# Performance work log

Hardware: AMD Instinct MI355X
Metric: run time of the kernel (lower is better)

The kernel has to match this reference:

```python
import jax, jax.numpy as jnp
import numpy as np

WS = 8          # window_size
NH = 4          # num_heads
C = 128         # embed_dim
HD = C // NH    # head_dim
HID = 4 * C     # mlp hidden
EPS = 1e-5


def _rel_pos_index(ws):
    coords = np.stack(np.meshgrid(np.arange(ws), np.arange(ws), indexing='ij')).reshape(2, -1)
    rel = coords[:, :, None] - coords[:, None, :]          # (2, N, N)
    rel = rel.transpose(1, 2, 0).astype(np.int64)          # (N, N, 2)
    rel[..., 0] += ws - 1
    rel[..., 1] += ws - 1
    rel[..., 0] *= 2 * ws - 1
    return rel.sum(-1)                                     # (N, N)


def _layernorm(x, g, b):
    mu = jnp.mean(x, axis=-1, keepdims=True)
    var = jnp.mean(jnp.square(x - mu), axis=-1, keepdims=True)
    return (x - mu) * jax.lax.rsqrt(var + EPS) * g + b


def setup_inputs() -> dict:
    key = jax.random.key(0)
    ks = jax.random.split(key, 12)
    B, L = 32, 4096
    s = 0.02
    return {
        'x': jax.random.normal(ks[0], (B, L, C), jnp.float32),
        'W_qkv': jax.random.normal(ks[1], (C, 3 * C), jnp.float32) * s,
        'b_qkv': jnp.zeros((3 * C,), jnp.float32),
        'W_out': jax.random.normal(ks[2], (C, C), jnp.float32) * s,
        'b_out': jnp.zeros((C,), jnp.float32),
        'bias_table': jax.random.normal(ks[3], ((2 * WS - 1) ** 2, NH), jnp.float32) * s,
        'g1': jnp.ones((C,), jnp.float32), 'be1': jnp.zeros((C,), jnp.float32),
        'g2': jnp.ones((C,), jnp.float32), 'be2': jnp.zeros((C,), jnp.float32),
        'W_fc1': jax.random.normal(ks[4], (C, HID), jnp.float32) * s,
        'b_fc1': jnp.zeros((HID,), jnp.float32),
        'W_fc2': jax.random.normal(ks[5], (HID, C), jnp.float32) * s,
        'b_fc2': jnp.zeros((C,), jnp.float32),
        'H': 64, 'W': 64,
    }


def reference(x, W_qkv, b_qkv, W_out, b_out, bias_table, g1, be1, g2, be2,
              W_fc1, b_fc1, W_fc2, b_fc2, H, W):
    B, L, _ = x.shape
    N = WS * WS
    shortcut = x
    xn = _layernorm(x, g1, be1)
    # window partition: (B,H,W,C) -> (B*nw, N, C)
    xw = xn.reshape(B, H // WS, WS, W // WS, WS, C)
    xw = xw.transpose(0, 1, 3, 2, 4, 5).reshape(-1, N, C)
    # attention
    qkv = (xw @ W_qkv + b_qkv).reshape(-1, N, 3, NH, HD)
    q, k, v = jnp.moveaxis(qkv, 2, 0)                      # each (Bw, N, NH, HD)
    attn = jnp.einsum('bnhd,bmhd->bhnm', q, k) * (HD ** -0.5)
    idx = jnp.asarray(_rel_pos_index(WS))                  # (N, N)
    bias = bias_table[idx].transpose(2, 0, 1)              # (NH, N, N)
    attn = jax.nn.softmax((attn + bias[None]).astype(jnp.float32), axis=-1).astype(x.dtype)
    o = jnp.einsum('bhnm,bmhd->bnhd', attn, v).reshape(-1, N, C)
    o = o @ W_out + b_out
    # window reverse
    o = o.reshape(B, H // WS, W // WS, WS, WS, C)
    o = o.transpose(0, 1, 3, 2, 4, 5).reshape(B, L, C)
    x = shortcut + o
    # MLP block
    xn = _layernorm(x, g2, be2)
    h = jax.nn.gelu(xn @ W_fc1 + b_fc1, approximate=False)
    return x + (h @ W_fc2 + b_fc2)
```

## Files before the change

### kernel.cpp

```cpp
#include <hip/hip_runtime.h>
#include <hip/hip_bf16.h>

typedef __bf16 bf16;
typedef __bf16 bf16x8 __attribute__((ext_vector_type(8)));
typedef __bf16 bf16x4 __attribute__((ext_vector_type(4)));
typedef float f32x4 __attribute__((ext_vector_type(4)));

#define C_DIM 128
#define LDA 136
#define LDQ 40
#define LDVT 72
#define LDP 72
#define LDH 264

__device__ __forceinline__ f32x4 mfma16(bf16x8 a, bf16x8 b, f32x4 c) {
  return __builtin_amdgcn_mfma_f32_16x16x32_bf16(a, b, c, 0, 0, 0);
}


__global__ __launch_bounds__(256, 2) void swin_fused(
    const float* __restrict__ x,
    const bf16*  __restrict__ Wqkv_t, const float* __restrict__ b_qkv,
    const bf16*  __restrict__ Wout_t, const float* __restrict__ b_out,
    const float* __restrict__ btabx,
    const float* __restrict__ g1, const float* __restrict__ be1,
    const float* __restrict__ g2, const float* __restrict__ be2,
    const bf16*  __restrict__ Wfc1_t, const float* __restrict__ b_fc1,
    const bf16*  __restrict__ Wfc2_t, const float* __restrict__ b_fc2,
    float* __restrict__ out)
{
  __shared__ __attribute__((aligned(16))) char smem[76800];
  bf16 (*sA)[LDA]       = (bf16(*)[LDA])(smem);
  bf16 (*sQ)[64][LDQ]   = (bf16(*)[64][LDQ])(smem + 17408);
  bf16 (*sK)[64][LDQ]   = (bf16(*)[64][LDQ])(smem + 37888);
  bf16 (*sVT)[32][LDVT] = (bf16(*)[32][LDVT])(smem + 58368);
  bf16 (*sP)[64][LDP]   = (bf16(*)[64][LDP])(smem + 17408);
  bf16 (*sY)[LDA]       = (bf16(*)[LDA])(smem + 17408);
  bf16 (*sH)[LDH]       = (bf16(*)[LDH])(smem + 17408);

  const int tid = threadIdx.x;
  const int w   = tid >> 6;
  const int l   = tid & 63;
  const int l15 = l & 15;
  const int lhi = l >> 4;

  const int win = blockIdx.x;
  const int b   = win >> 6;
  const int wy  = (win >> 3) & 7;
  const int wx  = win & 7;
  const int rowbase = b * 4096 + wy * 512 + wx * 8;

  f32x4 yreg[2][4];

  {
    const int tok = tid >> 2, seg = tid & 3;
    const int t = rowbase + (tok >> 3) * 64 + (tok & 7);
    const float* xr = x + (size_t)t * C_DIM + seg * 32;
    float f[32]; float s = 0.f, s2 = 0.f;
    #pragma unroll
    for (int i = 0; i < 8; i++) {
      f32x4 v = *(const f32x4*)(xr + i * 4);
      #pragma unroll
      for (int j = 0; j < 4; j++) { float a = v[j]; f[i*4+j] = a; s += a; s2 += a*a; }
    }
    s  += __shfl_xor(s, 1);  s  += __shfl_xor(s, 2);
    s2 += __shfl_xor(s2, 1); s2 += __shfl_xor(s2, 2);
    float mu = s * (1.f/128.f);
    float rs = rsqrtf(s2 * (1.f/128.f) - mu*mu + 1e-5f);
    #pragma unroll
    for (int i = 0; i < 4; i++) {
      f32x4 gv0 = *(const f32x4*)(g1  + seg*32 + i*8);
      f32x4 gv1 = *(const f32x4*)(g1  + seg*32 + i*8 + 4);
      f32x4 bv0 = *(const f32x4*)(be1 + seg*32 + i*8);
      f32x4 bv1 = *(const f32x4*)(be1 + seg*32 + i*8 + 4);
      bf16x8 o;
      #pragma unroll
      for (int j = 0; j < 4; j++) {
        o[j]   = (bf16)((f[i*8+j]   - mu) * rs * gv0[j] + bv0[j]);
        o[j+4] = (bf16)((f[i*8+j+4] - mu) * rs * gv1[j] + bv1[j]);
      }
      *(bf16x8*)&sA[tok][seg*32 + i*8] = o;
    }
  }
  __syncthreads();

  {
    bf16x8 a[4][4];
    #pragma unroll
    for (int mt = 0; mt < 4; mt++)
      #pragma unroll
      for (int ks = 0; ks < 4; ks++)
        a[mt][ks] = *(const bf16x8*)&sA[mt*16 + l15][ks*32 + lhi*8];
    const float scale = 0.17677669529663687f;
    #pragma unroll
    for (int nti = 0; nti < 6; nti++) {
      const int kind  = nti >> 1;
      const int dhalf = nti & 1;
      const int colg_l = kind*128 + w*32 + dhalf*16 + l15;
      const bf16* wp = Wqkv_t + (size_t)colg_l * 128 + lhi * 8;
      bf16x8 bw[4];
      #pragma unroll
      for (int ks = 0; ks < 4; ks++) bw[ks] = *(const bf16x8*)(wp + ks * 32);
      const int colg_o = kind*128 + w*32 + dhalf*16 + lhi*4;
      f32x4 bias4 = *(const f32x4*)(b_qkv + colg_o);
      const int d_base = dhalf*16 + lhi*4;
      #pragma unroll
      for (int mt = 0; mt < 4; mt++) {
        f32x4 acc = {0.f, 0.f, 0.f, 0.f};
        #pragma unroll
        for (int ks = 0; ks < 4; ks++) acc = mfma16(bw[ks], a[mt][ks], acc);
        const int token = mt*16 + l15;
        if (kind == 0) {
          bf16x4 v4;
          #pragma unroll
          for (int r = 0; r < 4; r++) v4[r] = (bf16)((acc[r] + bias4[r]) * scale);
          *(bf16x4*)&sQ[w][token][d_base] = v4;
        } else if (kind == 1) {
          bf16x4 v4;
          #pragma unroll
          for (int r = 0; r < 4; r++) v4[r] = (bf16)(acc[r] + bias4[r]);
          *(bf16x4*)&sK[w][token][d_base] = v4;
        } else {
          #pragma unroll
          for (int r = 0; r < 4; r++) sVT[w][d_base + r][token] = (bf16)(acc[r] + bias4[r]);
        }
      }
    }
  }

  {
    const int h = w;
    bf16x8 qf[4], kf[4];
    #pragma unroll
    for (int ctq = 0; ctq < 4; ctq++) qf[ctq] = *(const bf16x8*)&sQ[h][ctq*16 + l15][lhi*8];
    #pragma unroll
    for (int kt = 0; kt < 4; kt++) kf[kt] = *(const bf16x8*)&sK[h][kt*16 + l15][lhi*8];
    f32x4 sc[4][4];
    #pragma unroll
    for (int ctq = 0; ctq < 4; ctq++)
      #pragma unroll
      for (int kt = 0; kt < 4; kt++) {
        f32x4 z = {0.f, 0.f, 0.f, 0.f};
        sc[ctq][kt] = mfma16(kf[kt], qf[ctq], z);
      }
    __syncthreads();
    #pragma unroll
    for (int ctq = 0; ctq < 4; ctq++) {
      const int q = ctq*16 + l15;
      float e[4][4]; float loc = 0.f;
      #pragma unroll
      for (int kt = 0; kt < 4; kt++) {
        f32x4 bt = *(const f32x4*)(btabx + (size_t)(((h*64 + q)*16 + kt*4 + lhi) << 2));
        #pragma unroll
        for (int r = 0; r < 4; r++) { e[kt][r] = __expf(sc[ctq][kt][r] + bt[r]); loc += e[kt][r]; }
      }
      loc += __shfl_xor(loc, 16);
      loc += __shfl_xor(loc, 32);
      const float inv = 1.f / loc;
      #pragma unroll
      for (int kt = 0; kt < 4; kt++) {
        bf16x4 p4;
        #pragma unroll
        for (int r = 0; r < 4; r++) p4[r] = (bf16)(e[kt][r] * inv);
        *(bf16x4*)&sP[h][q][kt*16 + lhi*4] = p4;
      }
    }
    f32x4 o_[2][4];
    #pragma unroll
    for (int c2 = 0; c2 < 2; c2++)
      #pragma unroll
      for (int ctq = 0; ctq < 4; ctq++) { f32x4 z = {0.f,0.f,0.f,0.f}; o_[c2][ctq] = z; }
    #pragma unroll
    for (int ks = 0; ks < 2; ks++) {
      bf16x8 vf[2], pq[4];
      #pragma unroll
      for (int c2 = 0; c2 < 2; c2++) vf[c2] = *(const bf16x8*)&sVT[h][c2*16 + l15][ks*32 + lhi*8];
      #pragma unroll
      for (int ctq = 0; ctq < 4; ctq++) pq[ctq] = *(const bf16x8*)&sP[h][ctq*16 + l15][ks*32 + lhi*8];
      #pragma unroll
      for (int c2 = 0; c2 < 2; c2++)
        #pragma unroll
        for (int ctq = 0; ctq < 4; ctq++) o_[c2][ctq] = mfma16(vf[c2], pq[ctq], o_[c2][ctq]);
    }
    #pragma unroll
    for (int c2 = 0; c2 < 2; c2++)
      #pragma unroll
      for (int ctq = 0; ctq < 4; ctq++) {
        bf16x4 o4;
        #pragma unroll
        for (int r = 0; r < 4; r++) o4[r] = (bf16)o_[c2][ctq][r];
        *(bf16x4*)&sA[ctq*16 + l15][h*32 + c2*16 + lhi*4] = o4;
      }
  }
  __syncthreads();

  {
    bf16x8 a[4][4];
    #pragma unroll
    for (int mt = 0; mt < 4; mt++)
      #pragma unroll
      for (int ks = 0; ks < 4; ks++)
        a[mt][ks] = *(const bf16x8*)&sA[mt*16 + l15][ks*32 + lhi*8];
    #pragma unroll
    for (int nto = 0; nto < 2; nto++) {
      const int col_l = (w*2 + nto) * 16 + l15;
      const bf16* wp = Wout_t + (size_t)col_l * 128 + lhi * 8;
      bf16x8 bw[4];
      #pragma unroll
      for (int ks = 0; ks < 4; ks++) bw[ks] = *(const bf16x8*)(wp + ks * 32);
      const int col_o = (w*2 + nto) * 16 + lhi*4;
      f32x4 bo4 = *(const f32x4*)(b_out + col_o);
      #pragma unroll
      for (int mt = 0; mt < 4; mt++) {
        f32x4 acc = {0.f, 0.f, 0.f, 0.f};
        #pragma unroll
        for (int ks = 0; ks < 4; ks++) acc = mfma16(bw[ks], a[mt][ks], acc);
        const int token = mt*16 + l15;
        const int t = rowbase + (token >> 3) * 64 + (token & 7);
        f32x4 xv = *(const f32x4*)(x + (size_t)t * C_DIM + col_o);
        f32x4 yv; bf16x4 y4;
        #pragma unroll
        for (int r = 0; r < 4; r++) { yv[r] = acc[r] + bo4[r] + xv[r]; y4[r] = (bf16)yv[r]; }
        yreg[nto][mt] = yv;
        *(bf16x4*)&sY[token][col_o] = y4;
      }
    }
  }
  __syncthreads();

  {
    const int tok = tid >> 2, seg = tid & 3;
    float f[32]; float s = 0.f, s2 = 0.f;
    #pragma unroll
    for (int i = 0; i < 4; i++) {
      bf16x8 v = *(const bf16x8*)&sY[tok][seg*32 + i*8];
      #pragma unroll
      for (int j = 0; j < 8; j++) { float a = (float)v[j]; f[i*8+j] = a; s += a; s2 += a*a; }
    }
    s  += __shfl_xor(s, 1);  s  += __shfl_xor(s, 2);
    s2 += __shfl_xor(s2, 1); s2 += __shfl_xor(s2, 2);
    float mu = s * (1.f/128.f);
    float rs = rsqrtf(s2 * (1.f/128.f) - mu*mu + 1e-5f);
    #pragma unroll
    for (int i = 0; i < 4; i++) {
      f32x4 gv0 = *(const f32x4*)(g2  + seg*32 + i*8);
      f32x4 gv1 = *(const f32x4*)(g2  + seg*32 + i*8 + 4);
      f32x4 bv0 = *(const f32x4*)(be2 + seg*32 + i*8);
      f32x4 bv1 = *(const f32x4*)(be2 + seg*32 + i*8 + 4);
      bf16x8 o;
      #pragma unroll
      for (int j = 0; j < 4; j++) {
        o[j]   = (bf16)((f[i*8+j]   - mu) * rs * gv0[j] + bv0[j]);
        o[j+4] = (bf16)((f[i*8+j+4] - mu) * rs * gv1[j] + bv1[j]);
      }
      *(bf16x8*)&sA[tok][seg*32 + i*8] = o;
    }
  }
  __syncthreads();

  {
    bf16x8 a[4][4];
    #pragma unroll
    for (int mt = 0; mt < 4; mt++)
      #pragma unroll
      for (int ks = 0; ks < 4; ks++)
        a[mt][ks] = *(const bf16x8*)&sA[mt*16 + l15][ks*32 + lhi*8];
    f32x4 accF[2][4];
    #pragma unroll
    for (int i = 0; i < 2; i++)
      #pragma unroll
      for (int mt = 0; mt < 4; mt++) { f32x4 z = {0.f,0.f,0.f,0.f}; accF[i][mt] = z; }

    #pragma unroll
    for (int hf = 0; hf < 2; hf++) {
      #pragma unroll
      for (int nti = 0; nti < 4; nti++) {
        const int ntg    = hf*16 + w*4 + nti;
        const int colh_l = ntg*16 + l15;
        const bf16* wp = Wfc1_t + (size_t)colh_l * 128 + lhi * 8;
        bf16x8 bw[4];
        #pragma unroll
        for (int ks = 0; ks < 4; ks++) bw[ks] = *(const bf16x8*)(wp + ks * 32);
        const int colh_o = ntg*16 + lhi*4;
        f32x4 bb4 = *(const f32x4*)(b_fc1 + colh_o);
        const int colloc_o = (w*4 + nti)*16 + lhi*4;
        #pragma unroll
        for (int mt = 0; mt < 4; mt++) {
          f32x4 acc = {0.f, 0.f, 0.f, 0.f};
          #pragma unroll
          for (int ks = 0; ks < 4; ks++) acc = mfma16(bw[ks], a[mt][ks], acc);
          const int token = mt*16 + l15;
          bf16x4 h4;
          #pragma unroll
          for (int r = 0; r < 4; r++) {
            float v = acc[r] + bb4[r];
            h4[r] = (bf16)(v / (1.f + __expf(-1.702f * v)));
          }
          *(bf16x4*)&sH[token][colloc_o] = h4;
        }
      }
      __syncthreads();
      #pragma unroll
      for (int ks = 0; ks < 8; ks++) {
        bf16x8 ah[4];
        #pragma unroll
        for (int mt = 0; mt < 4; mt++) ah[mt] = *(const bf16x8*)&sH[mt*16 + l15][ks*32 + lhi*8];
        #pragma unroll
        for (int nto = 0; nto < 2; nto++) {
          bf16x8 bw2 = *(const bf16x8*)(Wfc2_t + (size_t)((w*2 + nto)*16 + l15) * 512 + hf*256 + ks*32 + lhi*8);
          #pragma unroll
          for (int mt = 0; mt < 4; mt++) accF[nto][mt] = mfma16(bw2, ah[mt], accF[nto][mt]);
        }
      }
      __syncthreads();
    }
    #pragma unroll
    for (int nto = 0; nto < 2; nto++) {
      const int col_o = (w*2 + nto)*16 + lhi*4;
      f32x4 bb = *(const f32x4*)(b_fc2 + col_o);
      #pragma unroll
      for (int mt = 0; mt < 4; mt++) {
        const int token = mt*16 + l15;
        const int t = rowbase + (token >> 3) * 64 + (token & 7);
        f32x4 ov;
        #pragma unroll
        for (int r = 0; r < 4; r++) ov[r] = accF[nto][mt][r] + bb[r] + yreg[nto][mt][r];
        *(f32x4*)(out + (size_t)t * C_DIM + col_o) = ov;
      }
    }
  }
}

__global__ void prep_transpose(
    const float* __restrict__ Wqkv, const float* __restrict__ Wout,
    const float* __restrict__ Wfc1, const float* __restrict__ Wfc2,
    const float* __restrict__ btab,
    bf16* __restrict__ Wqkv_t, bf16* __restrict__ Wout_t,
    bf16* __restrict__ Wfc1_t, bf16* __restrict__ Wfc2_t,
    float* __restrict__ btabx)
{
  int i = blockIdx.x * 256 + threadIdx.x;
  if (i < 49152) { int n = i >> 7, k = i & 127; Wqkv_t[i] = (bf16)Wqkv[k*384 + n]; return; }
  i -= 49152;
  if (i < 16384) { int n = i >> 7, k = i & 127; Wout_t[i] = (bf16)Wout[k*128 + n]; return; }
  i -= 16384;
  if (i < 65536) { int n = i >> 7, k = i & 127; Wfc1_t[i] = (bf16)Wfc1[k*512 + n]; return; }
  i -= 65536;
  if (i < 65536) { int n = i >> 9, k = i & 511; Wfc2_t[i] = (bf16)Wfc2[k*128 + n]; return; }
  i -= 65536;
  if (i < 16384) {
    int r   = i & 3;
    int lhi = (i >> 2) & 3;
    int kt  = (i >> 4) & 3;
    int q   = (i >> 6) & 63;
    int h   = i >> 12;
    int k = kt*16 + lhi*4 + r;
    int nr = q >> 3, nc = q & 7, mr = k >> 3, mc = k & 7;
    int idx = (nr - mr + 7) * 15 + (nc - mc + 7);
    btabx[i] = btab[idx * 4 + h];
  }
}

extern "C" void kernel_launch(void* const* d_in, const int* in_sizes, int n_in,
                              void* d_out, int out_size, void* d_ws, size_t ws_size,
                              hipStream_t stream)
{
  const float* x    = (const float*)d_in[0];
  const float* Wqkv = (const float*)d_in[1];
  const float* bqkv = (const float*)d_in[2];
  const float* Wout = (const float*)d_in[3];
  const float* bout = (const float*)d_in[4];
  const float* btab = (const float*)d_in[5];
  const float* g1   = (const float*)d_in[6];
  const float* be1  = (const float*)d_in[7];
  const float* g2   = (const float*)d_in[8];
  const float* be2  = (const float*)d_in[9];
  const float* Wfc1 = (const float*)d_in[10];
  const float* bfc1 = (const float*)d_in[11];
  const float* Wfc2 = (const float*)d_in[12];
  const float* bfc2 = (const float*)d_in[13];

  bf16* ws = (bf16*)d_ws;
  bf16* Wqkv_t = ws;
  bf16* Wout_t = ws + 49152;
  bf16* Wfc1_t = ws + 65536;
  bf16* Wfc2_t = ws + 131072;
  float* btabx = (float*)(ws + 196608);

  prep_transpose<<<832, 256, 0, stream>>>(Wqkv, Wout, Wfc1, Wfc2, btab,
                                          Wqkv_t, Wout_t, Wfc1_t, Wfc2_t, btabx);

  const int B = in_sizes[0] / (4096 * 128);
  swin_fused<<<dim3(B * 64), 256, 0, stream>>>(
      x, Wqkv_t, bqkv, Wout_t, bout, btabx, g1, be1, g2, be2,
      Wfc1_t, bfc1, Wfc2_t, bfc2, (float*)d_out);
}
```

Baseline: 172.4 us.

## Repartition post-attention stages per-wave by token rows to drop block barriers

The out-projection, LayerNorm2 and MLP stages now split work so each wave owns 16 tokens across all output columns, instead of each wave owning column slices for all 64 tokens. LayerNorm2 is computed straight from the MFMA accumulators using cross-lane shuffles. Intermediates go into per-wave private shared-memory buffers, which removes the block-wide __syncthreads between these stages. In exchange, every wave now streams the full Wout/Wfc1/Wfc2 weight matrices from global/L2, which is four times the per-wave weight traffic. The residual y is also kept only in bf16 for the final add.

New measurement: 343.9 us. 1.99x slower.

```diff
diff --git a/kernel.cpp b/kernel.cpp
--- a/kernel.cpp
+++ b/kernel.cpp
@@ -11,7 +11,6 @@
 #define LDQ 40
 #define LDVT 72
 #define LDP 72
-#define LDH 264
 
 __device__ __forceinline__ f32x4 mfma16(bf16x8 a, bf16x8 b, f32x4 c) {
   return __builtin_amdgcn_mfma_f32_16x16x32_bf16(a, b, c, 0, 0, 0);
@@ -35,8 +34,6 @@
   bf16 (*sK)[64][LDQ]   = (bf16(*)[64][LDQ])(smem + 37888);
   bf16 (*sVT)[32][LDVT] = (bf16(*)[32][LDVT])(smem + 58368);
   bf16 (*sP)[64][LDP]   = (bf16(*)[64][LDP])(smem + 17408);
-  bf16 (*sY)[LDA]       = (bf16(*)[LDA])(smem + 17408);
-  bf16 (*sH)[LDH]       = (bf16(*)[LDH])(smem + 17408);
 
   const int tid = threadIdx.x;
   const int w   = tid >> 6;
@@ -44,13 +41,14 @@
   const int l15 = l & 15;
   const int lhi = l >> 4;
 
+  bf16 (*xn2w)[130] = (bf16(*)[130])(smem + 17408 + w * 12480);
+  bf16 (*sHw)[260]  = (bf16(*)[260])(smem + 17408 + w * 12480 + 4160);
+
   const int win = blockIdx.x;
   const int b   = win >> 6;
   const int wy  = (win >> 3) & 7;
   const int wx  = win & 7;
   const int rowbase = b * 4096 + wy * 512 + wx * 8;
-
-  f32x4 yreg[2][4];
 
   {
     const int tok = tid >> 2, seg = tid & 3;
@@ -194,139 +192,98 @@
   }
   __syncthreads();
 
-  {
-    bf16x8 a[4][4];
-    #pragma unroll
-    for (int mt = 0; mt < 4; mt++)
-      #pragma unroll
-      for (int ks = 0; ks < 4; ks++)
-        a[mt][ks] = *(const bf16x8*)&sA[mt*16 + l15][ks*32 + lhi*8];
-    #pragma unroll
-    for (int nto = 0; nto < 2; nto++) {
-      const int col_l = (w*2 + nto) * 16 + l15;
-      const bf16* wp = Wout_t + (size_t)col_l * 128 + lhi * 8;
+  const int token = w*16 + l15;
+  const int t_g   = rowbase + (token >> 3) * 64 + (token & 7);
+
+  bf16x4 yb[8];
+
+  {
+    bf16x8 a4[4];
+    #pragma unroll
+    for (int ks = 0; ks < 4; ks++)
+      a4[ks] = *(const bf16x8*)&sA[w*16 + l15][ks*32 + lhi*8];
+    float s = 0.f, s2 = 0.f;
+    #pragma unroll
+    for (int nt = 0; nt < 8; nt++) {
+      const bf16* wp = Wout_t + (size_t)(nt*16 + l15) * 128 + lhi * 8;
       bf16x8 bw[4];
       #pragma unroll
       for (int ks = 0; ks < 4; ks++) bw[ks] = *(const bf16x8*)(wp + ks * 32);
-      const int col_o = (w*2 + nto) * 16 + lhi*4;
-      f32x4 bo4 = *(const f32x4*)(b_out + col_o);
-      #pragma unroll
-      for (int mt = 0; mt < 4; mt++) {
-        f32x4 acc = {0.f, 0.f, 0.f, 0.f};
-        #pragma unroll
-        for (int ks = 0; ks < 4; ks++) acc = mfma16(bw[ks], a[mt][ks], acc);
-        const int token = mt*16 + l15;
-        const int t = rowbase + (token >> 3) * 64 + (token & 7);
-        f32x4 xv = *(const f32x4*)(x + (size_t)t * C_DIM + col_o);
-        f32x4 yv; bf16x4 y4;
-        #pragma unroll
-        for (int r = 0; r < 4; r++) { yv[r] = acc[r] + bo4[r] + xv[r]; y4[r] = (bf16)yv[r]; }
-        yreg[nto][mt] = yv;
-        *(bf16x4*)&sY[token][col_o] = y4;
-      }
-    }
-  }
-  __syncthreads();
-
-  {
-    const int tok = tid >> 2, seg = tid & 3;
-    float f[32]; float s = 0.f, s2 = 0.f;
-    #pragma unroll
-    for (int i = 0; i < 4; i++) {
-      bf16x8 v = *(const bf16x8*)&sY[tok][seg*32 + i*8];
-      #pragma unroll
-      for (int j = 0; j < 8; j++) { float a = (float)v[j]; f[i*8+j] = a; s += a; s2 += a*a; }
-    }
-    s  += __shfl_xor(s, 1);  s  += __shfl_xor(s, 2);
-    s2 += __shfl_xor(s2, 1); s2 += __shfl_xor(s2, 2);
+      f32x4 bo4 = *(const f32x4*)(b_out + nt*16 + lhi*4);
+      f32x4 acc = {0.f, 0.f, 0.f, 0.f};
+      #pragma unroll
+      for (int ks = 0; ks < 4; ks++) acc = mfma16(bw[ks], a4[ks], acc);
+      f32x4 xv = *(const f32x4*)(x + (size_t)t_g * C_DIM + nt*16 + lhi*4);
+      #pragma unroll
+      for (int r = 0; r < 4; r++) {
+        float v = acc[r] + bo4[r] + xv[r];
+        s += v; s2 += v*v;
+        yb[nt][r] = (bf16)v;
+      }
+    }
+    s  += __shfl_xor(s, 16);  s  += __shfl_xor(s, 32);
+    s2 += __shfl_xor(s2, 16); s2 += __shfl_xor(s2, 32);
     float mu = s * (1.f/128.f);
     float rs = rsqrtf(s2 * (1.f/128.f) - mu*mu + 1e-5f);
     #pragma unroll
-    for (int i = 0; i < 4; i++) {
-      f32x4 gv0 = *(const f32x4*)(g2  + seg*32 + i*8);
-      f32x4 gv1 = *(const f32x4*)(g2  + seg*32 + i*8 + 4);
-      f32x4 bv0 = *(const f32x4*)(be2 + seg*32 + i*8);
-      f32x4 bv1 = *(const f32x4*)(be2 + seg*32 + i*8 + 4);
-      bf16x8 o;
-      #pragma unroll
-      for (int j = 0; j < 4; j++) {
-        o[j]   = (bf16)((f[i*8+j]   - mu) * rs * gv0[j] + bv0[j]);
-        o[j+4] = (bf16)((f[i*8+j+4] - mu) * rs * gv1[j] + bv1[j]);
-      }
-      *(bf16x8*)&sA[tok][seg*32 + i*8] = o;
-    }
-  }
-  __syncthreads();
-
-  {
-    bf16x8 a[4][4];
-    #pragma unroll
-    for (int mt = 0; mt < 4; mt++)
-      #pragma unroll
-      for (int ks = 0; ks < 4; ks++)
-        a[mt][ks] = *(const bf16x8*)&sA[mt*16 + l15][ks*32 + lhi*8];
-    f32x4 accF[2][4];
-    #pragma unroll
-    for (int i = 0; i < 2; i++)
-      #pragma unroll
-      for (int mt = 0; mt < 4; mt++) { f32x4 z = {0.f,0.f,0.f,0.f}; accF[i][mt] = z; }
+    for (int nt = 0; nt < 8; nt++) {
+      f32x4 gv = *(const f32x4*)(g2  + nt*16 + lhi*4);
+      f32x4 bv = *(const f32x4*)(be2 + nt*16 + lhi*4);
+      bf16x4 x2;
+      #pragma unroll
+      for (int r = 0; r < 4; r++)
+        x2[r] = (bf16)(((float)yb[nt][r] - mu) * rs * gv[r] + bv[r]);
+      *(bf16x4*)&xn2w[l15][nt*16 + lhi*4] = x2;
+    }
+  }
+
+  {
+    bf16x8 a6[4];
+    #pragma unroll
+    for (int ks = 0; ks < 4; ks++)
+      a6[ks] = *(const bf16x8*)&xn2w[l15][ks*32 + lhi*8];
+    f32x4 accF[8];
+    #pragma unroll
+    for (int nt = 0; nt < 8; nt++) { f32x4 z = {0.f,0.f,0.f,0.f}; accF[nt] = z; }
 
     #pragma unroll
     for (int hf = 0; hf < 2; hf++) {
       #pragma unroll
-      for (int nti = 0; nti < 4; nti++) {
-        const int ntg    = hf*16 + w*4 + nti;
-        const int colh_l = ntg*16 + l15;
-        const bf16* wp = Wfc1_t + (size_t)colh_l * 128 + lhi * 8;
+      for (int ntl = 0; ntl < 16; ntl++) {
+        const int ntg = hf*16 + ntl;
+        const bf16* wp = Wfc1_t + (size_t)(ntg*16 + l15) * 128 + lhi * 8;
         bf16x8 bw[4];
         #pragma unroll
         for (int ks = 0; ks < 4; ks++) bw[ks] = *(const bf16x8*)(wp + ks * 32);
-        const int colh_o = ntg*16 + lhi*4;
-        f32x4 bb4 = *(const f32x4*)(b_fc1 + colh_o);
-        const int colloc_o = (w*4 + nti)*16 + lhi*4;
-        #pragma unroll
-        for (int mt = 0; mt < 4; mt++) {
-          f32x4 acc = {0.f, 0.f, 0.f, 0.f};
-          #pragma unroll
-          for (int ks = 0; ks < 4; ks++) acc = mfma16(bw[ks], a[mt][ks], acc);
-          const int token = mt*16 + l15;
-          bf16x4 h4;
-          #pragma unroll
-          for (int r = 0; r < 4; r++) {
-            float v = acc[r] + bb4[r];
-            h4[r] = (bf16)(v / (1.f + __expf(-1.702f * v)));
-          }
-          *(bf16x4*)&sH[token][colloc_o] = h4;
+        f32x4 bb4 = *(const f32x4*)(b_fc1 + ntg*16 + lhi*4);
+        f32x4 acc = {0.f, 0.f, 0.f, 0.f};
+        #pragma unroll
+        for (int ks = 0; ks < 4; ks++) acc = mfma16(bw[ks], a6[ks], acc);
+        bf16x4 h4;
+        #pragma unroll
+        for (int r = 0; r < 4; r++) {
+          float v = acc[r] + bb4[r];
+          h4[r] = (bf16)(v / (1.f + __expf(-1.702f * v)));
         }
-      }
-      __syncthreads();
-      #pragma unroll
-      for (int ks = 0; ks < 8; ks++) {
-        bf16x8 ah[4];
-        #pragma unroll
-        for (int mt = 0; mt < 4; mt++) ah[mt] = *(const bf16x8*)&sH[mt*16 + l15][ks*32 + lhi*8];
-        #pragma unroll
-        for (int nto = 0; nto < 2; nto++) {
-          bf16x8 bw2 = *(const bf16x8*)(Wfc2_t + (size_t)((w*2 + nto)*16 + l15) * 512 + hf*256 + ks*32 + lhi*8);
-          #pragma unroll
-          for (int mt = 0; mt < 4; mt++) accF[nto][mt] = mfma16(bw2, ah[mt], accF[nto][mt]);
+        *(bf16x4*)&sHw[l15][ntl*16 + lhi*4] = h4;
+      }
+      #pragma unroll
+      for (int ks8 = 0; ks8 < 8; ks8++) {
+        bf16x8 ah = *(const bf16x8*)&sHw[l15][ks8*32 + lhi*8];
+        #pragma unroll
+        for (int nt = 0; nt < 8; nt++) {
+          bf16x8 bw2 = *(const bf16x8*)(Wfc2_t + (size_t)(nt*16 + l15) * 512 + hf*256 + ks8*32 + lhi*8);
+          accF[nt] = mfma16(bw2, ah, accF[nt]);
         }
       }
-      __syncthreads();
-    }
-    #pragma unroll
-    for (int nto = 0; nto < 2; nto++) {
-      const int col_o = (w*2 + nto)*16 + lhi*4;
-      f32x4 bb = *(const f32x4*)(b_fc2 + col_o);
-      #pragma unroll
-      for (int mt = 0; mt < 4; mt++) {
-        const int token = mt*16 + l15;
-        const int t = rowbase + (token >> 3) * 64 + (token & 7);
-        f32x4 ov;
-        #pragma unroll
-        for (int r = 0; r < 4; r++) ov[r] = accF[nto][mt][r] + bb[r] + yreg[nto][mt][r];
-        *(f32x4*)(out + (size_t)t * C_DIM + col_o) = ov;
-      }
+    }
+    #pragma unroll
+    for (int nt = 0; nt < 8; nt++) {
+      f32x4 bb = *(const f32x4*)(b_fc2 + nt*16 + lhi*4);
+      f32x4 ov;
+      #pragma unroll
+      for (int r = 0; r < 4; r++) ov[r] = accF[nt][r] + bb[r] + (float)yb[nt][r];
+      *(f32x4*)(out + (size_t)t_g * C_DIM + nt*16 + lhi*4) = ov;
     }
   }
 }
```
